# Performance work log

Hardware: AMD Instinct MI355X
Metric: run time of the kernel (lower is better)

## Reference

```python
import jax, jax.numpy as jnp
import numpy as np

B, D, R, E = 16384, 512, 64, 8

def setup_inputs() -> dict:
    key = jax.random.key(0)
    ks = jax.random.split(key, 8)
    return {
        "x0": jax.random.normal(ks[0], (B, D), jnp.float32),
        "x": jax.random.normal(ks[1], (B, D), jnp.float32),
        "U": jax.random.normal(ks[2], (E, D, R), jnp.float32) * 0.02,
        "V": jax.random.normal(ks[3], (E, R, D), jnp.float32) * 0.02,
        "C": jax.random.normal(ks[4], (E, R, R), jnp.float32) * 0.02,
        "b": jnp.zeros((E, D), jnp.float32),
        "Wg": jax.random.normal(ks[5], (E, D), jnp.float32) * 0.02,
        "bg": jnp.zeros((E,), jnp.float32),
    }

def reference(x0, x, U, V, C, b, Wg, bg):
    # gate: softmax over experts
    g = jax.nn.softmax(x @ Wg.T + bg, axis=1)            # [B, E]
    # per-expert low-rank bilinear transform, batched over experts
    xv = jnp.einsum('bd,erd->ber', x, V)                 # x @ V[e].T
    xvc = jnp.einsum('ber,ers->bes', xv, C)              # xv @ C[e]
    proj = jnp.einsum('bes,eds->bed', xvc, U)            # xvc @ U[e].T
    # gated sum: sum_e g_e * (x0*proj_e + b_e + x)
    gproj = jnp.einsum('be,bed->bd', g, proj)
    out = x0 * gproj + g @ b + x * g.sum(axis=1, keepdims=True)
    return out
```

## Files before the change

kernel.cpp:

```cpp
#include <hip/hip_runtime.h>
#include <math.h>


typedef __bf16 bf16_t;
typedef __attribute__((ext_vector_type(8))) __bf16 bf16x8;
typedef __attribute__((ext_vector_type(4))) __bf16 bf16x4;
typedef __attribute__((ext_vector_type(4))) float  floatx4;

__device__ __forceinline__ void async16(void* lds, const void* gp) {
  __builtin_amdgcn_global_load_lds(
      (__attribute__((address_space(1))) void*)(gp),
      (__attribute__((address_space(3))) void*)(lds), 16, 0, 0);
}

__global__ __launch_bounds__(256) void prep_kernel(
    const float* __restrict__ U, const float* __restrict__ V, const float* __restrict__ C,
    bf16_t* __restrict__ VCc, bf16_t* __restrict__ Ut) {
  int tid = blockIdx.x * 256 + threadIdx.x;
  if (tid < 512 * 512) {
    int n = tid >> 9, d = tid & 511;
    int e = n >> 6, s = n & 63;
    const float* Vp = V + (size_t)e * 64 * 512 + d;
    const float* Cp = C + (size_t)e * 64 * 64 + s;
    float acc = 0.f;
#pragma unroll 8
    for (int r = 0; r < 64; ++r) acc += Vp[(size_t)r * 512] * Cp[r * 64];
    VCc[tid] = (bf16_t)acc;
  } else {
    int i2 = tid - 512 * 512;
    int d = i2 >> 9, n = i2 & 511;
    int e = n >> 6, s = n & 63;
    Ut[i2] = (bf16_t)U[((size_t)e * 512 + d) * 64 + s];
  }
}

__global__ __launch_bounds__(256) void gate_kernel(
    const float* __restrict__ x, const float* __restrict__ Wg, const float* __restrict__ bg,
    bf16_t* __restrict__ xbf, float* __restrict__ g) {
  int wave = threadIdx.x >> 6, lane = threadIdx.x & 63;
  int row = blockIdx.x * 4 + wave;
  const float4* xr = (const float4*)(x + (size_t)row * 512);
  float4 v0 = xr[lane];
  float4 v1 = xr[lane + 64];
  bf16x4* xb = (bf16x4*)(xbf + (size_t)row * 512);
  bf16x4 b0, b1;
  b0.x = (bf16_t)v0.x; b0.y = (bf16_t)v0.y; b0.z = (bf16_t)v0.z; b0.w = (bf16_t)v0.w;
  b1.x = (bf16_t)v1.x; b1.y = (bf16_t)v1.y; b1.z = (bf16_t)v1.z; b1.w = (bf16_t)v1.w;
  xb[lane] = b0;
  xb[lane + 64] = b1;
  float acc[8];
#pragma unroll
  for (int e = 0; e < 8; ++e) {
    const float4* wp = (const float4*)(Wg + (size_t)e * 512);
    float4 w0 = wp[lane], w1 = wp[lane + 64];
    acc[e] = v0.x * w0.x + v0.y * w0.y + v0.z * w0.z + v0.w * w0.w +
             v1.x * w1.x + v1.y * w1.y + v1.z * w1.z + v1.w * w1.w;
  }
#pragma unroll
  for (int e = 0; e < 8; ++e) {
#pragma unroll
    for (int off = 32; off > 0; off >>= 1) acc[e] += __shfl_xor(acc[e], off, 64);
  }
  float z[8], mx = -1e30f;
#pragma unroll
  for (int e = 0; e < 8; ++e) { z[e] = acc[e] + bg[e]; mx = fmaxf(mx, z[e]); }
  float s = 0.f;
#pragma unroll
  for (int e = 0; e < 8; ++e) { z[e] = __expf(z[e] - mx); s += z[e]; }
  float inv = 1.f / s;
  if (lane == 0) {
#pragma unroll
    for (int e = 0; e < 8; ++e) g[(size_t)row * 8 + e] = z[e] * inv;
  }
}

__device__ __forceinline__ void gemm_core(
    const bf16_t* __restrict__ A, const bf16_t* __restrict__ Bt,
    int m0, int n0, int t, floatx4 acc[4][4]) {
  __shared__ char lds[32768];
  char* ldsA = lds;
  char* ldsB = lds + 16384;
  const int wave = t >> 6, lane = t & 63;
  const int wr = wave >> 1, wc = wave & 1;
  const int lhi = lane >> 4, llo = lane & 15;
#pragma unroll 1
  for (int it = 0; it < 8; ++it) {
    const int k0 = it * 64;
    __syncthreads();
#pragma unroll
    for (int i = 0; i < 4; ++i) {
      int c = i * 256 + t;
      int r = c >> 3, q = c & 7;
      int p = q ^ (r & 7);
      const char* ga = (const char*)A + (size_t)(m0 + r) * 1024 + k0 * 2 + p * 16;
      async16(ldsA + (i * 256 + wave * 64) * 16, ga);
      const char* gb = (const char*)Bt + (size_t)(n0 + r) * 1024 + k0 * 2 + p * 16;
      async16(ldsB + (i * 256 + wave * 64) * 16, gb);
    }
    __syncthreads();
#pragma unroll
    for (int ks = 0; ks < 2; ++ks) {
      bf16x8 af[4], bfm[4];
#pragma unroll
      for (int i = 0; i < 4; ++i) {
        int rA = wr * 64 + i * 16 + llo;
        af[i]  = *(const bf16x8*)(ldsA + rA * 128 + (((ks * 4 + lhi) ^ (rA & 7)) << 4));
        int rB = wc * 64 + i * 16 + llo;
        bfm[i] = *(const bf16x8*)(ldsB + rB * 128 + (((ks * 4 + lhi) ^ (rB & 7)) << 4));
      }
#pragma unroll
      for (int i = 0; i < 4; ++i)
#pragma unroll
        for (int j = 0; j < 4; ++j)
          acc[i][j] = __builtin_amdgcn_mfma_f32_16x16x32_bf16(af[i], bfm[j], acc[i][j], 0, 0, 0);
    }
  }
}

__global__ __launch_bounds__(256, 2) void gemm1_kernel(
    const bf16_t* __restrict__ xbf, const bf16_t* __restrict__ VCc,
    const float* __restrict__ g, bf16_t* __restrict__ T) {
  int t = threadIdx.x;
  int m0 = blockIdx.x * 128, n0 = blockIdx.y * 128;
  floatx4 acc[4][4];
#pragma unroll
  for (int i = 0; i < 4; ++i)
#pragma unroll
    for (int j = 0; j < 4; ++j) acc[i][j] = (floatx4){0.f, 0.f, 0.f, 0.f};
  gemm_core(xbf, VCc, m0, n0, t, acc);
  const int wave = t >> 6, lane = t & 63;
  const int wr = wave >> 1, wc = wave & 1;
  const int lhi = lane >> 4, llo = lane & 15;
  const int e = (n0 + wc * 64) >> 6;
#pragma unroll
  for (int i = 0; i < 4; ++i) {
#pragma unroll
    for (int r = 0; r < 4; ++r) {
      int m = m0 + wr * 64 + i * 16 + lhi * 4 + r;
      float gv = g[(size_t)m * 8 + e];
#pragma unroll
      for (int j = 0; j < 4; ++j) {
        int n = n0 + wc * 64 + j * 16 + llo;
        T[(size_t)m * 512 + n] = (bf16_t)(acc[i][j][r] * gv);
      }
    }
  }
}

__global__ __launch_bounds__(256, 2) void gemm2_kernel(
    const bf16_t* __restrict__ T, const bf16_t* __restrict__ Ut,
    const float* __restrict__ g, const float* __restrict__ bvec,
    const float* __restrict__ x0, const float* __restrict__ x,
    float* __restrict__ out) {
  int t = threadIdx.x;
  int m0 = blockIdx.x * 128, n0 = blockIdx.y * 128;
  floatx4 acc[4][4];
#pragma unroll
  for (int i = 0; i < 4; ++i)
#pragma unroll
    for (int j = 0; j < 4; ++j) acc[i][j] = (floatx4){0.f, 0.f, 0.f, 0.f};
  gemm_core(T, Ut, m0, n0, t, acc);
  const int wave = t >> 6, lane = t & 63;
  const int wr = wave >> 1, wc = wave & 1;
  const int lhi = lane >> 4, llo = lane & 15;
  float bb4[4][8];
#pragma unroll
  for (int j = 0; j < 4; ++j) {
    int n = n0 + wc * 64 + j * 16 + llo;
#pragma unroll
    for (int e = 0; e < 8; ++e) bb4[j][e] = bvec[(size_t)e * 512 + n];
  }
#pragma unroll
  for (int i = 0; i < 4; ++i) {
#pragma unroll
    for (int r = 0; r < 4; ++r) {
      int m = m0 + wr * 64 + i * 16 + lhi * 4 + r;
      float g8[8], gsum = 0.f;
#pragma unroll
      for (int e = 0; e < 8; ++e) { g8[e] = g[(size_t)m * 8 + e]; gsum += g8[e]; }
#pragma unroll
      for (int j = 0; j < 4; ++j) {
        int n = n0 + wc * 64 + j * 16 + llo;
        float bias = 0.f;
#pragma unroll
        for (int e = 0; e < 8; ++e) bias += g8[e] * bb4[j][e];
        size_t idx = (size_t)m * 512 + n;
        out[idx] = x0[idx] * acc[i][j][r] + bias + x[idx] * gsum;
      }
    }
  }
}

extern "C" void kernel_launch(void* const* d_in, const int* in_sizes, int n_in,
                              void* d_out, int out_size, void* d_ws, size_t ws_size,
                              hipStream_t stream) {
  const float* x0 = (const float*)d_in[0];
  const float* x  = (const float*)d_in[1];
  const float* U  = (const float*)d_in[2];
  const float* V  = (const float*)d_in[3];
  const float* C  = (const float*)d_in[4];
  const float* bv = (const float*)d_in[5];
  const float* Wg = (const float*)d_in[6];
  const float* bg = (const float*)d_in[7];
  float* out = (float*)d_out;

  char* ws = (char*)d_ws;
  bf16_t* xbf = (bf16_t*)(ws);
  bf16_t* T   = (bf16_t*)(ws + 16777216);
  bf16_t* VCc = (bf16_t*)(ws + 33554432);
  bf16_t* Ut  = (bf16_t*)(ws + 34078720);
  float*  g   = (float*)(ws + 34603008);

  prep_kernel<<<2048, 256, 0, stream>>>(U, V, C, VCc, Ut);
  gate_kernel<<<4096, 256, 0, stream>>>(x, Wg, bg, xbf, g);
  gemm1_kernel<<<dim3(128, 4), 256, 0, stream>>>(xbf, VCc, g, T);
  gemm2_kernel<<<dim3(128, 4), 256, 0, stream>>>(T, Ut, g, bv, x0, x, out);
}
```

Before: 165.2 us.

## Stage full-K B panel in LDS and stream A fragments directly from global

Both GEMMs now use 128x64 tiles, which doubles the grid to 1024 blocks. Each block copies the whole 64x512 B panel (full K) into 64 KB of swizzled LDS once. After that, each wave reads its A rows straight from global memory into registers, so the per-K-step LDS staging loop and its barriers are gone. The epilogues stage g and bias in LDS instead of loading them repeatedly from global. In exchange, each block uses 64 KB of LDS (which may limit blocks per CU), A loads go through uncached per-lane global reads with no double buffering, and the larger grid loads A twice as many times.

Result: slower. 179.4 us (+8.6%).

```diff
diff --git a/kernel.cpp b/kernel.cpp
--- a/kernel.cpp
+++ b/kernel.cpp
@@ -6,12 +6,6 @@
 typedef __attribute__((ext_vector_type(8))) __bf16 bf16x8;
 typedef __attribute__((ext_vector_type(4))) __bf16 bf16x4;
 typedef __attribute__((ext_vector_type(4))) float  floatx4;
-
-__device__ __forceinline__ void async16(void* lds, const void* gp) {
-  __builtin_amdgcn_global_load_lds(
-      (__attribute__((address_space(1))) void*)(gp),
-      (__attribute__((address_space(3))) void*)(lds), 16, 0, 0);
-}
 
 __global__ __launch_bounds__(256) void prep_kernel(
     const float* __restrict__ U, const float* __restrict__ V, const float* __restrict__ C,
@@ -74,45 +68,37 @@
   }
 }
 
-__device__ __forceinline__ void gemm_core(
+__device__ __forceinline__ void gemm_stream(
     const bf16_t* __restrict__ A, const bf16_t* __restrict__ Bt,
-    int m0, int n0, int t, floatx4 acc[4][4]) {
-  __shared__ char lds[32768];
-  char* ldsA = lds;
-  char* ldsB = lds + 16384;
-  const int wave = t >> 6, lane = t & 63;
-  const int wr = wave >> 1, wc = wave & 1;
+    char* ldsB, int m0, int n0, int t, floatx4 acc[2][4]) {
+  {
+    const float4* src = (const float4*)(Bt + (size_t)n0 * 512);
+#pragma unroll
+    for (int i = 0; i < 16; ++i) {
+      int G = i * 256 + t;
+      int n = G >> 6, c = G & 63;
+      *(float4*)(ldsB + n * 1024 + ((c ^ (n & 7)) << 4)) = src[G];
+    }
+  }
+  __syncthreads();
+  const int lane = t & 63, wave = t >> 6;
   const int lhi = lane >> 4, llo = lane & 15;
-#pragma unroll 1
-  for (int it = 0; it < 8; ++it) {
-    const int k0 = it * 64;
-    __syncthreads();
-#pragma unroll
-    for (int i = 0; i < 4; ++i) {
-      int c = i * 256 + t;
-      int r = c >> 3, q = c & 7;
-      int p = q ^ (r & 7);
-      const char* ga = (const char*)A + (size_t)(m0 + r) * 1024 + k0 * 2 + p * 16;
-      async16(ldsA + (i * 256 + wave * 64) * 16, ga);
-      const char* gb = (const char*)Bt + (size_t)(n0 + r) * 1024 + k0 * 2 + p * 16;
-      async16(ldsB + (i * 256 + wave * 64) * 16, gb);
-    }
-    __syncthreads();
-#pragma unroll
-    for (int ks = 0; ks < 2; ++ks) {
-      bf16x8 af[4], bfm[4];
-#pragma unroll
-      for (int i = 0; i < 4; ++i) {
-        int rA = wr * 64 + i * 16 + llo;
-        af[i]  = *(const bf16x8*)(ldsA + rA * 128 + (((ks * 4 + lhi) ^ (rA & 7)) << 4));
-        int rB = wc * 64 + i * 16 + llo;
-        bfm[i] = *(const bf16x8*)(ldsB + rB * 128 + (((ks * 4 + lhi) ^ (rB & 7)) << 4));
-      }
-#pragma unroll
-      for (int i = 0; i < 4; ++i)
-#pragma unroll
-        for (int j = 0; j < 4; ++j)
-          acc[i][j] = __builtin_amdgcn_mfma_f32_16x16x32_bf16(af[i], bfm[j], acc[i][j], 0, 0, 0);
+  const char* pA0 = (const char*)A + (size_t)(m0 + wave * 32 + llo) * 1024 + lhi * 16;
+  const char* pA1 = pA0 + 16 * 1024;
+  const char* pB = ldsB + llo * 1024;
+  const int bsw = (llo & 7) << 4;
+#pragma unroll 4
+  for (int ks = 0; ks < 16; ++ks) {
+    bf16x8 a0 = *(const bf16x8*)(pA0 + ks * 64);
+    bf16x8 a1 = *(const bf16x8*)(pA1 + ks * 64);
+    bf16x8 bf[4];
+#pragma unroll
+    for (int nf = 0; nf < 4; ++nf)
+      bf[nf] = *(const bf16x8*)(pB + nf * 16 * 1024 + ((((ks * 4 + lhi) << 4) ^ bsw)));
+#pragma unroll
+    for (int nf = 0; nf < 4; ++nf) {
+      acc[0][nf] = __builtin_amdgcn_mfma_f32_16x16x32_bf16(a0, bf[nf], acc[0][nf], 0, 0, 0);
+      acc[1][nf] = __builtin_amdgcn_mfma_f32_16x16x32_bf16(a1, bf[nf], acc[1][nf], 0, 0, 0);
     }
   }
 }
@@ -120,29 +106,31 @@
 __global__ __launch_bounds__(256, 2) void gemm1_kernel(
     const bf16_t* __restrict__ xbf, const bf16_t* __restrict__ VCc,
     const float* __restrict__ g, bf16_t* __restrict__ T) {
-  int t = threadIdx.x;
-  int m0 = blockIdx.x * 128, n0 = blockIdx.y * 128;
-  floatx4 acc[4][4];
-#pragma unroll
-  for (int i = 0; i < 4; ++i)
+  __shared__ char lds[65536];
+  const int t = threadIdx.x;
+  const int m0 = blockIdx.x * 128, n0 = blockIdx.y * 64;
+  floatx4 acc[2][4];
+#pragma unroll
+  for (int i = 0; i < 2; ++i)
 #pragma unroll
     for (int j = 0; j < 4; ++j) acc[i][j] = (floatx4){0.f, 0.f, 0.f, 0.f};
-  gemm_core(xbf, VCc, m0, n0, t, acc);
-  const int wave = t >> 6, lane = t & 63;
-  const int wr = wave >> 1, wc = wave & 1;
+  gemm_stream(xbf, VCc, lds, m0, n0, t, acc);
+  __syncthreads();
+  float* gcol = (float*)lds;
+  if (t < 128) gcol[t] = g[(size_t)(m0 + t) * 8 + (n0 >> 6)];
+  __syncthreads();
+  const int lane = t & 63, wave = t >> 6;
   const int lhi = lane >> 4, llo = lane & 15;
-  const int e = (n0 + wc * 64) >> 6;
-#pragma unroll
-  for (int i = 0; i < 4; ++i) {
+#pragma unroll
+  for (int mf = 0; mf < 2; ++mf) {
 #pragma unroll
     for (int r = 0; r < 4; ++r) {
-      int m = m0 + wr * 64 + i * 16 + lhi * 4 + r;
-      float gv = g[(size_t)m * 8 + e];
-#pragma unroll
-      for (int j = 0; j < 4; ++j) {
-        int n = n0 + wc * 64 + j * 16 + llo;
-        T[(size_t)m * 512 + n] = (bf16_t)(acc[i][j][r] * gv);
-      }
+      int rml = wave * 32 + mf * 16 + lhi * 4 + r;
+      float gv = gcol[rml];
+      size_t mrow = (size_t)(m0 + rml) * 512;
+#pragma unroll
+      for (int nf = 0; nf < 4; ++nf)
+        T[mrow + n0 + nf * 16 + llo] = (bf16_t)(acc[mf][nf][r] * gv);
     }
   }
 }
@@ -152,40 +140,49 @@
     const float* __restrict__ g, const float* __restrict__ bvec,
     const float* __restrict__ x0, const float* __restrict__ x,
     float* __restrict__ out) {
-  int t = threadIdx.x;
-  int m0 = blockIdx.x * 128, n0 = blockIdx.y * 128;
-  floatx4 acc[4][4];
-#pragma unroll
-  for (int i = 0; i < 4; ++i)
+  __shared__ char lds[65536];
+  const int t = threadIdx.x;
+  const int m0 = blockIdx.x * 128, n0 = blockIdx.y * 64;
+  floatx4 acc[2][4];
+#pragma unroll
+  for (int i = 0; i < 2; ++i)
 #pragma unroll
     for (int j = 0; j < 4; ++j) acc[i][j] = (floatx4){0.f, 0.f, 0.f, 0.f};
-  gemm_core(T, Ut, m0, n0, t, acc);
-  const int wave = t >> 6, lane = t & 63;
-  const int wr = wave >> 1, wc = wave & 1;
+  gemm_stream(T, Ut, lds, m0, n0, t, acc);
+  __syncthreads();
+  float* ldsG = (float*)lds;
+  float* ldsBv = (float*)(lds + 4096);
+  ((float4*)ldsG)[t] = ((const float4*)(g + (size_t)m0 * 8))[t];
+  if (t < 128)
+    ((float4*)ldsBv)[t] = ((const float4*)bvec)[(t >> 4) * 128 + (n0 >> 2) + (t & 15)];
+  __syncthreads();
+  const int lane = t & 63, wave = t >> 6;
   const int lhi = lane >> 4, llo = lane & 15;
-  float bb4[4][8];
-#pragma unroll
-  for (int j = 0; j < 4; ++j) {
-    int n = n0 + wc * 64 + j * 16 + llo;
-#pragma unroll
-    for (int e = 0; e < 8; ++e) bb4[j][e] = bvec[(size_t)e * 512 + n];
-  }
-#pragma unroll
-  for (int i = 0; i < 4; ++i) {
+  float bb[4][8];
+#pragma unroll
+  for (int nf = 0; nf < 4; ++nf) {
+    int nl = nf * 16 + llo;
+#pragma unroll
+    for (int e = 0; e < 8; ++e) bb[nf][e] = ldsBv[e * 64 + nl];
+  }
+#pragma unroll
+  for (int mf = 0; mf < 2; ++mf) {
 #pragma unroll
     for (int r = 0; r < 4; ++r) {
-      int m = m0 + wr * 64 + i * 16 + lhi * 4 + r;
-      float g8[8], gsum = 0.f;
-#pragma unroll
-      for (int e = 0; e < 8; ++e) { g8[e] = g[(size_t)m * 8 + e]; gsum += g8[e]; }
-#pragma unroll
-      for (int j = 0; j < 4; ++j) {
-        int n = n0 + wc * 64 + j * 16 + llo;
+      int rml = wave * 32 + mf * 16 + lhi * 4 + r;
+      float4 ga = ((const float4*)ldsG)[rml * 2];
+      float4 gb2 = ((const float4*)ldsG)[rml * 2 + 1];
+      float g8[8] = {ga.x, ga.y, ga.z, ga.w, gb2.x, gb2.y, gb2.z, gb2.w};
+      float gsum = g8[0] + g8[1] + g8[2] + g8[3] + g8[4] + g8[5] + g8[6] + g8[7];
+      size_t mrow = (size_t)(m0 + rml) * 512;
+#pragma unroll
+      for (int nf = 0; nf < 4; ++nf) {
+        int n = n0 + nf * 16 + llo;
         float bias = 0.f;
 #pragma unroll
-        for (int e = 0; e < 8; ++e) bias += g8[e] * bb4[j][e];
-        size_t idx = (size_t)m * 512 + n;
-        out[idx] = x0[idx] * acc[i][j][r] + bias + x[idx] * gsum;
+        for (int e = 0; e < 8; ++e) bias += g8[e] * bb[nf][e];
+        size_t idx = mrow + n;
+        out[idx] = x0[idx] * acc[mf][nf][r] + bias + x[idx] * gsum;
       }
     }
   }
@@ -213,6 +210,6 @@
 
   prep_kernel<<<2048, 256, 0, stream>>>(U, V, C, VCc, Ut);
   gate_kernel<<<4096, 256, 0, stream>>>(x, Wg, bg, xbf, g);
-  gemm1_kernel<<<dim3(128, 4), 256, 0, stream>>>(xbf, VCc, g, T);
-  gemm2_kernel<<<dim3(128, 4), 256, 0, stream>>>(T, Ut, g, bv, x0, x, out);
-}
+  gemm1_kernel<<<dim3(128, 8), 256, 0, stream>>>(xbf, VCc, g, T);
+  gemm2_kernel<<<dim3(128, 8), 256, 0, stream>>>(T, Ut, g, bv, x0, x, out);
+}
```
